# Kernel optimization log

Hardware: AMD Instinct MI355X
Metric: run time of the kernel (lower is better)

Reference implementation:

```python
import jax, jax.numpy as jnp
import numpy as np

D_MODEL = 512
NHEAD = 8
HEAD_DIM = D_MODEL // NHEAD
A, B = 1024, 16


def setup_inputs() -> dict:
    key = jax.random.key(0)
    ks = jax.random.split(key, 6)
    s = 1.0 / np.sqrt(D_MODEL)
    return {
        "src": jax.random.normal(ks[0], (A, B, D_MODEL), jnp.float32),
        "asset_relation_bias": jax.random.normal(ks[1], (A, A), jnp.float32) * 0.1,
        "Wq": jax.random.normal(ks[2], (D_MODEL, D_MODEL), jnp.float32) * s,
        "bq": jnp.zeros((D_MODEL,), jnp.float32),
        "Wk": jax.random.normal(ks[3], (D_MODEL, D_MODEL), jnp.float32) * s,
        "bk": jnp.zeros((D_MODEL,), jnp.float32),
        "Wv": jax.random.normal(ks[4], (D_MODEL, D_MODEL), jnp.float32) * s,
        "bv": jnp.zeros((D_MODEL,), jnp.float32),
        "Wo": jax.random.normal(ks[5], (D_MODEL, D_MODEL), jnp.float32) * s,
        "bo": jnp.zeros((D_MODEL,), jnp.float32),
    }


def reference(src, asset_relation_bias, Wq, bq, Wk, bk, Wv, bv, Wo, bo):
    # src: [A, B, H]; attention is over the asset dim A.
    scale = HEAD_DIM ** -0.5

    def proj_heads(x, W, b):
        y = x @ W.T + b                      # [A, B, H]  (torch Linear: x @ W.T + b)
        y = y.reshape(A, B, NHEAD, HEAD_DIM)
        return jnp.transpose(y, (1, 2, 0, 3))  # [B, nh, A, hd]

    q = proj_heads(src, Wq, bq)
    k = proj_heads(src, Wk, bk)
    v = proj_heads(src, Wv, bv)

    logits = jnp.einsum("bnad,bnkd->bnak", q, k) * scale  # [B, nh, A, A]
    logits = logits + asset_relation_bias[None, None]     # additive relation bias
    attn = jax.nn.softmax(logits, axis=-1)                # dropout = identity (eval)
    out = jnp.einsum("bnak,bnkd->bnad", attn, v)          # [B, nh, A, hd]
    out = jnp.transpose(out, (2, 0, 1, 3)).reshape(A, B, D_MODEL)
    out = out @ Wo.T + bo
    return out
```

## Files before the change

kernel.cpp:

```cpp
#include <hip/hip_runtime.h>
#include <hip/hip_bf16.h>

#define A_DIM 1024
#define B_DIM 16
#define DM    512
#define NH    8
#define HD    64

#define LDT 72

typedef short s16x8 __attribute__((ext_vector_type(8)));
typedef float f32x4 __attribute__((ext_vector_type(4)));

static __device__ __forceinline__ unsigned short f2b(float f) {
    __hip_bfloat16 h = __float2bfloat16(f);
    unsigned short u;
    __builtin_memcpy(&u, &h, 2);
    return u;
}
static __device__ __forceinline__ uint2 cvt4(float4 v) {
    __hip_bfloat162 lo = __float22bfloat162_rn(make_float2(v.x, v.y));
    __hip_bfloat162 hi = __float22bfloat162_rn(make_float2(v.z, v.w));
    unsigned int ulo, uhi;
    __builtin_memcpy(&ulo, &lo, 4);
    __builtin_memcpy(&uhi, &hi, 4);
    return make_uint2(ulo, uhi);
}

static __device__ __forceinline__ void gl_lds16(const short* g, short* l) {
    __builtin_amdgcn_global_load_lds(
        (const __attribute__((address_space(1))) unsigned int*)g,
        (__attribute__((address_space(3))) unsigned int*)l, 16, 0, 0);
}

__global__ __launch_bounds__(256) void cvt_src(
    const float* __restrict__ in, short* __restrict__ out)
{
    int i = (blockIdx.x * 256 + threadIdx.x) * 8;
    float4 a = *(const float4*)&in[i];
    float4 b = *(const float4*)&in[i + 4];
    *(uint2*)&out[i]     = cvt4(a);
    *(uint2*)&out[i + 4] = cvt4(b);
}

__global__ __launch_bounds__(256) void cvt_w(
    const float* __restrict__ Wq, const float* __restrict__ Wk,
    const float* __restrict__ Wv, const float* __restrict__ Wo,
    short* __restrict__ Wall)
{
    int i = blockIdx.x * 256 + threadIdx.x;
    int mat = i >> 15;
    const float* W = (mat == 0) ? Wq : (mat == 1) ? Wk : (mat == 2) ? Wv : Wo;
    int j = (i & 32767) * 8;
    float4 a = *(const float4*)&W[j];
    float4 b = *(const float4*)&W[j + 4];
    *(uint2*)&Wall[mat * (DM * DM) + j]     = cvt4(a);
    *(uint2*)&Wall[mat * (DM * DM) + j + 4] = cvt4(b);
}

__global__ __launch_bounds__(256) void qkv_gemm_bf(
    const short* __restrict__ Sb, const short* __restrict__ Wall,
    const float* __restrict__ bq, const float* __restrict__ bk,
    const float* __restrict__ bv,
    short* __restrict__ Qb, short* __restrict__ Kb, short* __restrict__ Vb)
{
    __shared__ __align__(16) short As[128 * 64];
    __shared__ __align__(16) short Bs[128 * 64];

    const int tid  = threadIdx.x;
    const int wave = tid >> 6, lane = tid & 63;
    const int quad = lane >> 4, l16 = lane & 15;
    const int waveM = (wave >> 1) * 64, waveN = (wave & 1) * 64;
    const int mbase = blockIdx.y * 128;
    const int nbase = blockIdx.x * 128;
    const int mat   = nbase >> 9;
    const short* Wm   = Wall + mat * (DM * DM);
    const float* bvec = (mat == 0) ? bq : (mat == 1) ? bk : bv;
    short* dst        = (mat == 0) ? Qb : (mat == 1) ? Kb : Vb;
    const float oscale = (mat == 0) ? 0.125f : 1.0f;
    const int wrow0 = nbase & 511;

    const int srow = lane >> 3;
    const int scol = (lane & 7) ^ srow;
    const int cxa  = l16 & 7;

    f32x4 acc[4][4];
    #pragma unroll
    for (int i = 0; i < 4; i++)
        #pragma unroll
        for (int j = 0; j < 4; j++)
            acc[i][j] = (f32x4){0.f, 0.f, 0.f, 0.f};

    for (int kb = 0; kb < 8; ++kb) {
        __syncthreads();
        #pragma unroll
        for (int p = 0; p < 4; p++) {
            int ch = wave + p * 4;
            int r  = ch * 8 + srow;
            gl_lds16(&Sb[(mbase + r) * 512 + kb * 64 + scol * 8],
                     &As[ch * 8 * 64]);
            gl_lds16(&Wm[(wrow0 + r) * 512 + kb * 64 + scol * 8],
                     &Bs[ch * 8 * 64]);
        }
        __syncthreads();
        #pragma unroll
        for (int k0i = 0; k0i < 2; k0i++) {
            s16x8 af[4], bf[4];
            #pragma unroll
            for (int mi = 0; mi < 4; mi++)
                af[mi] = *(const s16x8*)&As[(waveM + mi * 16 + l16) * 64
                                            + (((k0i * 4 + quad) ^ cxa) * 8)];
            #pragma unroll
            for (int ni = 0; ni < 4; ni++)
                bf[ni] = *(const s16x8*)&Bs[(waveN + ni * 16 + l16) * 64
                                            + (((k0i * 4 + quad) ^ cxa) * 8)];
            #pragma unroll
            for (int mi = 0; mi < 4; mi++)
                #pragma unroll
                for (int ni = 0; ni < 4; ni++)
                    acc[mi][ni] = __builtin_amdgcn_mfma_f32_16x16x32_bf16(
                        af[mi], bf[ni], acc[mi][ni], 0, 0, 0);
        }
    }

    #pragma unroll
    for (int mi = 0; mi < 4; mi++) {
        #pragma unroll
        for (int ni = 0; ni < 4; ni++) {
            #pragma unroll
            for (int r = 0; r < 4; r++) {
                int t = mbase + waveM + mi * 16 + quad * 4 + r;
                int o = wrow0 + waveN + ni * 16 + l16;
                float v = (acc[mi][ni][r] + bvec[o]) * oscale;
                int a = t >> 4, bb = t & 15, n = o >> 6, d = o & 63;
                dst[((bb * NH + n) * A_DIM + a) * HD + d] = (short)f2b(v);
            }
        }
    }
}

__global__ __launch_bounds__(256) void qkv_gemm(
    const float* __restrict__ src,
    const float* __restrict__ Wq, const float* __restrict__ bq,
    const float* __restrict__ Wk, const float* __restrict__ bk,
    const float* __restrict__ Wv, const float* __restrict__ bv,
    short* __restrict__ Qb, short* __restrict__ Kb, short* __restrict__ Vb)
{
    __shared__ short As[128 * LDT];
    __shared__ short Bs[128 * LDT];

    const int tid  = threadIdx.x;
    const int wave = tid >> 6, lane = tid & 63;
    const int quad = lane >> 4, l16 = lane & 15;
    const int waveM = (wave >> 1) * 64, waveN = (wave & 1) * 64;
    const int mbase = blockIdx.y * 128;
    const int nbase = blockIdx.x * 128;
    const int mat   = nbase >> 9;
    const float* W    = (mat == 0) ? Wq : (mat == 1) ? Wk : Wv;
    const float* bvec = (mat == 0) ? bq : (mat == 1) ? bk : bv;
    short* dst        = (mat == 0) ? Qb : (mat == 1) ? Kb : Vb;
    const float oscale = (mat == 0) ? 0.125f : 1.0f;
    const int wrow0 = nbase & 511;

    f32x4 acc[4][4];
    #pragma unroll
    for (int i = 0; i < 4; i++)
        #pragma unroll
        for (int j = 0; j < 4; j++)
            acc[i][j] = (f32x4){0.f, 0.f, 0.f, 0.f};

    for (int kb = 0; kb < 8; ++kb) {
        __syncthreads();
        #pragma unroll
        for (int p = 0; p < 8; p++) {
            int chunk = tid + p * 256;
            int row = chunk >> 4, c = chunk & 15;
            float4 a4 = *(const float4*)&src[(mbase + row) * 512 + kb * 64 + c * 4];
            *(uint2*)&As[row * LDT + c * 4] = cvt4(a4);
            float4 w4 = *(const float4*)&W[(wrow0 + row) * 512 + kb * 64 + c * 4];
            *(uint2*)&Bs[row * LDT + c * 4] = cvt4(w4);
        }
        __syncthreads();
        #pragma unroll
        for (int k0i = 0; k0i < 2; k0i++) {
            s16x8 af[4], bf[4];
            #pragma unroll
            for (int mi = 0; mi < 4; mi++)
                af[mi] = *(const s16x8*)&As[(waveM + mi * 16 + l16) * LDT + (k0i * 4 + quad) * 8];
            #pragma unroll
            for (int ni = 0; ni < 4; ni++)
                bf[ni] = *(const s16x8*)&Bs[(waveN + ni * 16 + l16) * LDT + (k0i * 4 + quad) * 8];
            #pragma unroll
            for (int mi = 0; mi < 4; mi++)
                #pragma unroll
                for (int ni = 0; ni < 4; ni++)
                    acc[mi][ni] = __builtin_amdgcn_mfma_f32_16x16x32_bf16(
                        af[mi], bf[ni], acc[mi][ni], 0, 0, 0);
        }
    }

    #pragma unroll
    for (int mi = 0; mi < 4; mi++) {
        #pragma unroll
        for (int ni = 0; ni < 4; ni++) {
            #pragma unroll
            for (int r = 0; r < 4; r++) {
                int t = mbase + waveM + mi * 16 + quad * 4 + r;
                int o = wrow0 + waveN + ni * 16 + l16;
                float v = (acc[mi][ni][r] + bvec[o]) * oscale;
                int a = t >> 4, bb = t & 15, n = o >> 6, d = o & 63;
                dst[((bb * NH + n) * A_DIM + a) * HD + d] = (short)f2b(v);
            }
        }
    }
}

__global__ __launch_bounds__(256) void attn_kernel(
    const short* __restrict__ Qb, const short* __restrict__ Kb,
    const short* __restrict__ Vb, const float* __restrict__ bias,
    short* __restrict__ AO)
{
    __shared__ short Ks[64 * LDT];
    __shared__ short Vt[64 * LDT];
    __shared__ short Ps[4][16 * LDT];

    const int tid  = threadIdx.x;
    const int wave = tid >> 6, lane = tid & 63;
    const int quad = lane >> 4, l16 = lane & 15;
    const int bn = blockIdx.y;
    const int qrow0 = blockIdx.x * 64 + wave * 16;

    const short* Qg = Qb + bn * (A_DIM * HD);
    const short* Kg = Kb + bn * (A_DIM * HD);
    const short* Vg = Vb + bn * (A_DIM * HD);

    s16x8 qf[2];
    #pragma unroll
    for (int k0i = 0; k0i < 2; k0i++)
        qf[k0i] = *(const s16x8*)&Qg[(qrow0 + l16) * HD + k0i * 32 + quad * 8];

    float lsum[4];
    f32x4 of[4];
    #pragma unroll
    for (int r = 0; r < 4; r++) lsum[r] = 0.f;
    #pragma unroll
    for (int db = 0; db < 4; db++) of[db] = (f32x4){0.f, 0.f, 0.f, 0.f};

    for (int kb = 0; kb < 16; ++kb) {
        __syncthreads();
        #pragma unroll
        for (int p = 0; p < 2; p++) {
            int chunk = tid + p * 256;
            int row = chunk >> 3, c = chunk & 7;
            *(s16x8*)&Ks[row * LDT + c * 8] =
                *(const s16x8*)&Kg[(kb * 64 + row) * HD + c * 8];
            s16x8 vv = *(const s16x8*)&Vg[(kb * 64 + row) * HD + c * 8];
            #pragma unroll
            for (int j = 0; j < 8; j++) {
                int d = c * 8 + j;
                Vt[d * LDT + (((row >> 3) ^ c) << 3) + (row & 7)] = vv[j];
            }
        }
        __syncthreads();

        float sv[4][4];
        #pragma unroll
        for (int cb = 0; cb < 4; cb++) {
            f32x4 s = (f32x4){0.f, 0.f, 0.f, 0.f};
            #pragma unroll
            for (int k0i = 0; k0i < 2; k0i++) {
                s16x8 kf = *(const s16x8*)&Ks[(cb * 16 + l16) * LDT + (k0i * 4 + quad) * 8];
                s = __builtin_amdgcn_mfma_f32_16x16x32_bf16(qf[k0i], kf, s, 0, 0, 0);
            }
            #pragma unroll
            for (int r = 0; r < 4; r++) {
                int arow = qrow0 + quad * 4 + r;
                int kcol = kb * 64 + cb * 16 + l16;
                sv[cb][r] = s[r] + bias[arow * A_DIM + kcol];
            }
        }

        #pragma unroll
        for (int r = 0; r < 4; r++) {
            int prow = quad * 4 + r;
            #pragma unroll
            for (int cb = 0; cb < 4; cb++) {
                float pv = __expf(sv[cb][r]);
                lsum[r] += pv;
                Ps[wave][prow * LDT + cb * 16 + l16] = (short)f2b(pv);
            }
        }

        #pragma unroll
        for (int k0i = 0; k0i < 2; k0i++) {
            s16x8 pf = *(const s16x8*)&Ps[wave][l16 * LDT + (k0i * 4 + quad) * 8];
            #pragma unroll
            for (int db = 0; db < 4; db++) {
                int rr = db * 16 + l16;
                s16x8 vf = *(const s16x8*)&Vt[rr * LDT +
                            (((k0i * 4 + quad) ^ (rr >> 3)) << 3)];
                of[db] = __builtin_amdgcn_mfma_f32_16x16x32_bf16(pf, vf, of[db], 0, 0, 0);
            }
        }
    }

    #pragma unroll
    for (int r = 0; r < 4; r++) {
        float ps = lsum[r];
        ps += __shfl_xor(ps, 1);
        ps += __shfl_xor(ps, 2);
        ps += __shfl_xor(ps, 4);
        ps += __shfl_xor(ps, 8);
        lsum[r] = 1.0f / ps;
    }

    const int b = bn >> 3, n = bn & 7;
    #pragma unroll
    for (int db = 0; db < 4; db++) {
        #pragma unroll
        for (int r = 0; r < 4; r++) {
            int a = qrow0 + quad * 4 + r;
            int d = db * 16 + l16;
            float v = of[db][r] * lsum[r];
            AO[(a * B_DIM + b) * DM + n * HD + d] = (short)f2b(v);
        }
    }
}

__global__ __launch_bounds__(256) void out_gemm_bf(
    const short* __restrict__ Xin,
    const short* __restrict__ Wob, const float* __restrict__ bo,
    float* __restrict__ out)
{
    __shared__ __align__(16) short As[128 * 64];
    __shared__ __align__(16) short Bs[128 * 64];

    const int tid  = threadIdx.x;
    const int wave = tid >> 6, lane = tid & 63;
    const int quad = lane >> 4, l16 = lane & 15;
    const int waveM = (wave >> 1) * 64, waveN = (wave & 1) * 64;
    const int mbase = blockIdx.y * 128;
    const int nbase = blockIdx.x * 128;

    const int srow = lane >> 3;
    const int scol = (lane & 7) ^ srow;
    const int cxa  = l16 & 7;

    f32x4 acc[4][4];
    #pragma unroll
    for (int i = 0; i < 4; i++)
        #pragma unroll
        for (int j = 0; j < 4; j++)
            acc[i][j] = (f32x4){0.f, 0.f, 0.f, 0.f};

    for (int kb = 0; kb < 8; ++kb) {
        __syncthreads();
        #pragma unroll
        for (int p = 0; p < 4; p++) {
            int ch = wave + p * 4;
            int r  = ch * 8 + srow;
            gl_lds16(&Xin[(mbase + r) * 512 + kb * 64 + scol * 8],
                     &As[ch * 8 * 64]);
            gl_lds16(&Wob[(nbase + r) * 512 + kb * 64 + scol * 8],
                     &Bs[ch * 8 * 64]);
        }
        __syncthreads();
        #pragma unroll
        for (int k0i = 0; k0i < 2; k0i++) {
            s16x8 af[4], bf[4];
            #pragma unroll
            for (int mi = 0; mi < 4; mi++)
                af[mi] = *(const s16x8*)&As[(waveM + mi * 16 + l16) * 64
                                            + (((k0i * 4 + quad) ^ cxa) * 8)];
            #pragma unroll
            for (int ni = 0; ni < 4; ni++)
                bf[ni] = *(const s16x8*)&Bs[(waveN + ni * 16 + l16) * 64
                                            + (((k0i * 4 + quad) ^ cxa) * 8)];
            #pragma unroll
            for (int mi = 0; mi < 4; mi++)
                #pragma unroll
                for (int ni = 0; ni < 4; ni++)
                    acc[mi][ni] = __builtin_amdgcn_mfma_f32_16x16x32_bf16(
                        af[mi], bf[ni], acc[mi][ni], 0, 0, 0);
        }
    }

    #pragma unroll
    for (int mi = 0; mi < 4; mi++) {
        #pragma unroll
        for (int ni = 0; ni < 4; ni++) {
            #pragma unroll
            for (int r = 0; r < 4; r++) {
                int t = mbase + waveM + mi * 16 + quad * 4 + r;
                int o = nbase + waveN + ni * 16 + l16;
                out[t * 512 + o] = acc[mi][ni][r] + bo[o];
            }
        }
    }
}

__global__ __launch_bounds__(256) void out_gemm(
    const short* __restrict__ Xin,
    const float* __restrict__ Wo, const float* __restrict__ bo,
    float* __restrict__ out)
{
    __shared__ short As[128 * LDT];
    __shared__ short Bs[128 * LDT];

    const int tid  = threadIdx.x;
    const int wave = tid >> 6, lane = tid & 63;
    const int quad = lane >> 4, l16 = lane & 15;
    const int waveM = (wave >> 1) * 64, waveN = (wave & 1) * 64;
    const int mbase = blockIdx.y * 128;
    const int nbase = blockIdx.x * 128;

    f32x4 acc[4][4];
    #pragma unroll
    for (int i = 0; i < 4; i++)
        #pragma unroll
        for (int j = 0; j < 4; j++)
            acc[i][j] = (f32x4){0.f, 0.f, 0.f, 0.f};

    for (int kb = 0; kb < 8; ++kb) {
        __syncthreads();
        #pragma unroll
        for (int p = 0; p < 4; p++) {
            int chunk = tid + p * 256;
            int row = chunk >> 3, c = chunk & 7;
            *(s16x8*)&As[row * LDT + c * 8] =
                *(const s16x8*)&Xin[(mbase + row) * 512 + kb * 64 + c * 8];
        }
        #pragma unroll
        for (int p = 0; p < 8; p++) {
            int chunk = tid + p * 256;
            int row = chunk >> 4, c = chunk & 15;
            float4 w4 = *(const float4*)&Wo[(nbase + row) * 512 + kb * 64 + c * 4];
            *(uint2*)&Bs[row * LDT + c * 4] = cvt4(w4);
        }
        __syncthreads();
        #pragma unroll
        for (int k0i = 0; k0i < 2; k0i++) {
            s16x8 af[4], bf[4];
            #pragma unroll
            for (int mi = 0; mi < 4; mi++)
                af[mi] = *(const s16x8*)&As[(waveM + mi * 16 + l16) * LDT + (k0i * 4 + quad) * 8];
            #pragma unroll
            for (int ni = 0; ni < 4; ni++)
                bf[ni] = *(const s16x8*)&Bs[(waveN + ni * 16 + l16) * LDT + (k0i * 4 + quad) * 8];
            #pragma unroll
            for (int mi = 0; mi < 4; mi++)
                #pragma unroll
                for (int ni = 0; ni < 4; ni++)
                    acc[mi][ni] = __builtin_amdgcn_mfma_f32_16x16x32_bf16(
                        af[mi], bf[ni], acc[mi][ni], 0, 0, 0);
        }
    }

    #pragma unroll
    for (int mi = 0; mi < 4; mi++) {
        #pragma unroll
        for (int ni = 0; ni < 4; ni++) {
            #pragma unroll
            for (int r = 0; r < 4; r++) {
                int t = mbase + waveM + mi * 16 + quad * 4 + r;
                int o = nbase + waveN + ni * 16 + l16;
                out[t * 512 + o] = acc[mi][ni][r] + bo[o];
            }
        }
    }
}

extern "C" void kernel_launch(void* const* d_in, const int* in_sizes, int n_in,
                              void* d_out, int out_size, void* d_ws, size_t ws_size,
                              hipStream_t stream) {
    const float* src  = (const float*)d_in[0];
    const float* bias = (const float*)d_in[1];
    const float* Wq   = (const float*)d_in[2];
    const float* bq   = (const float*)d_in[3];
    const float* Wk   = (const float*)d_in[4];
    const float* bk   = (const float*)d_in[5];
    const float* Wv   = (const float*)d_in[6];
    const float* bv   = (const float*)d_in[7];
    const float* Wo   = (const float*)d_in[8];
    const float* bo   = (const float*)d_in[9];

    short* ws = (short*)d_ws;
    short* Qb = ws;
    short* Kb = ws + (size_t)(1 << 23);
    short* Vb = ws + (size_t)(2 << 23);

    const bool big2   = ws_size >= (size_t)(66u << 20);
    const bool big_ws = ws_size >= (size_t)(64u << 20);

    if (big2) {
        short* Sb   = ws + (size_t)3 * (1 << 23);
        short* Wall = ws + (size_t)4 * (1 << 23);
        short* AO   = Sb;

        cvt_src<<<dim3(4096), 256, 0, stream>>>(src, Sb);
        cvt_w<<<dim3(512), 256, 0, stream>>>(Wq, Wk, Wv, Wo, Wall);
        qkv_gemm_bf<<<dim3(12, 128), 256, 0, stream>>>(Sb, Wall, bq, bk, bv, Qb, Kb, Vb);
        attn_kernel<<<dim3(16, 128), 256, 0, stream>>>(Qb, Kb, Vb, bias, AO);
        out_gemm_bf<<<dim3(4, 128), 256, 0, stream>>>(AO, Wall + 3 * (DM * DM), bo,
                                                      (float*)d_out);
    } else {
        short* AO = big_ws ? (ws + (size_t)3 * (1 << 23))
                           : (short*)d_out;

        qkv_gemm<<<dim3(12, 128), 256, 0, stream>>>(src, Wq, bq, Wk, bk, Wv, bv, Qb, Kb, Vb);
        attn_kernel<<<dim3(16, 128), 256, 0, stream>>>(Qb, Kb, Vb, bias, AO);

        if (big_ws) {
            out_gemm<<<dim3(4, 128), 256, 0, stream>>>(AO, Wo, bo, (float*)d_out);
        } else {
            float* Cs = (float*)d_ws;
            out_gemm<<<dim3(4, 128), 256, 0, stream>>>(AO, Wo, bo, Cs);
            (void)hipMemcpyAsync(d_out, Cs, (size_t)out_size * sizeof(float),
                                 hipMemcpyDeviceToDevice, stream);
        }
    }
}
```

Before: 241.8 us.

## Pre-transpose V and double-buffer K/V tiles in attention kernel

Adds a v_tr kernel that transposes V into a [bn, d, a] layout, using the output buffer as scratch. A new attention kernel reads the transposed V and double-buffers K and V shared-memory tiles. The next tile is prefetched into registers while the current one is computed, so there is one barrier per iteration. This aims to hide global load latency and simplify V staging, at the cost of an extra launch and a full extra read and write of V.

```diff
diff --git a/kernel.cpp b/kernel.cpp
--- a/kernel.cpp
+++ b/kernel.cpp
@@ -56,6 +56,30 @@
     float4 b = *(const float4*)&W[j + 4];
     *(uint2*)&Wall[mat * (DM * DM) + j]     = cvt4(a);
     *(uint2*)&Wall[mat * (DM * DM) + j + 4] = cvt4(b);
+}
+
+__global__ __launch_bounds__(256) void v_tr(
+    const short* __restrict__ V, short* __restrict__ Vt)
+{
+    __shared__ short t[64][74];
+    const int bn = blockIdx.y, a0 = blockIdx.x * 64;
+    const int rr = threadIdx.x >> 3, c = threadIdx.x & 7;
+
+    #pragma unroll
+    for (int h = 0; h < 2; h++) {
+        int a = rr + h * 32;
+        *(s16x8*)&t[a][c * 8] =
+            *(const s16x8*)&V[((size_t)bn * A_DIM + a0 + a) * HD + c * 8];
+    }
+    __syncthreads();
+    #pragma unroll
+    for (int h = 0; h < 2; h++) {
+        int d = rr + h * 32;
+        s16x8 y;
+        #pragma unroll
+        for (int j = 0; j < 8; j++) y[j] = t[c * 8 + j][d];
+        *(s16x8*)&Vt[((size_t)bn * HD + d) * A_DIM + a0 + c * 8] = y;
+    }
 }
 
 __global__ __launch_bounds__(256) void qkv_gemm_bf(
@@ -211,6 +235,138 @@
                 int a = t >> 4, bb = t & 15, n = o >> 6, d = o & 63;
                 dst[((bb * NH + n) * A_DIM + a) * HD + d] = (short)f2b(v);
             }
+        }
+    }
+}
+
+__global__ __launch_bounds__(256) void attn_kernel2(
+    const short* __restrict__ Qb, const short* __restrict__ Kb,
+    const short* __restrict__ Vtg, const float* __restrict__ bias,
+    short* __restrict__ AO)
+{
+    __shared__ short Ks[2][64 * LDT];
+    __shared__ short Vt[2][64 * LDT];
+    __shared__ short Ps[4][16 * LDT];
+
+    const int tid  = threadIdx.x;
+    const int wave = tid >> 6, lane = tid & 63;
+    const int quad = lane >> 4, l16 = lane & 15;
+    const int bn = blockIdx.y;
+    const int qrow0 = blockIdx.x * 64 + wave * 16;
+
+    const short* Qg = Qb  + bn * (A_DIM * HD);
+    const short* Kg = Kb  + bn * (A_DIM * HD);
+    const short* Vg = Vtg + bn * (HD * A_DIM);
+
+    s16x8 qf[2];
+    #pragma unroll
+    for (int k0i = 0; k0i < 2; k0i++)
+        qf[k0i] = *(const s16x8*)&Qg[(qrow0 + l16) * HD + k0i * 32 + quad * 8];
+
+    const int srow = tid >> 3, sc = tid & 7;
+
+    float lsum[4];
+    f32x4 of[4];
+    #pragma unroll
+    for (int r = 0; r < 4; r++) lsum[r] = 0.f;
+    #pragma unroll
+    for (int db = 0; db < 4; db++) of[db] = (f32x4){0.f, 0.f, 0.f, 0.f};
+
+    s16x8 kpre[2], vpre[2];
+    #pragma unroll
+    for (int p = 0; p < 2; p++) {
+        kpre[p] = *(const s16x8*)&Kg[(srow + p * 32) * HD + sc * 8];
+        vpre[p] = *(const s16x8*)&Vg[(srow + p * 32) * A_DIM + sc * 8];
+    }
+    #pragma unroll
+    for (int p = 0; p < 2; p++) {
+        int row = srow + p * 32;
+        *(s16x8*)&Ks[0][row * LDT + sc * 8] = kpre[p];
+        *(s16x8*)&Vt[0][row * LDT + ((sc ^ (wave + p * 4)) << 3)] = vpre[p];
+    }
+
+    int cur = 0;
+    for (int kb = 0; kb < 16; ++kb) {
+        __syncthreads();
+
+        if (kb < 15) {
+            #pragma unroll
+            for (int p = 0; p < 2; p++) {
+                kpre[p] = *(const s16x8*)&Kg[((kb + 1) * 64 + srow + p * 32) * HD + sc * 8];
+                vpre[p] = *(const s16x8*)&Vg[(srow + p * 32) * A_DIM + (kb + 1) * 64 + sc * 8];
+            }
+        }
+
+        float sv[4][4];
+        #pragma unroll
+        for (int cb = 0; cb < 4; cb++) {
+            f32x4 s = (f32x4){0.f, 0.f, 0.f, 0.f};
+            #pragma unroll
+            for (int k0i = 0; k0i < 2; k0i++) {
+                s16x8 kf = *(const s16x8*)&Ks[cur][(cb * 16 + l16) * LDT + (k0i * 4 + quad) * 8];
+                s = __builtin_amdgcn_mfma_f32_16x16x32_bf16(qf[k0i], kf, s, 0, 0, 0);
+            }
+            #pragma unroll
+            for (int r = 0; r < 4; r++) {
+                int arow = qrow0 + quad * 4 + r;
+                int kcol = kb * 64 + cb * 16 + l16;
+                sv[cb][r] = s[r] + bias[arow * A_DIM + kcol];
+            }
+        }
+
+        #pragma unroll
+        for (int r = 0; r < 4; r++) {
+            int prow = quad * 4 + r;
+            #pragma unroll
+            for (int cb = 0; cb < 4; cb++) {
+                float pv = __expf(sv[cb][r]);
+                lsum[r] += pv;
+                Ps[wave][prow * LDT + cb * 16 + l16] = (short)f2b(pv);
+            }
+        }
+
+        #pragma unroll
+        for (int k0i = 0; k0i < 2; k0i++) {
+            s16x8 pf = *(const s16x8*)&Ps[wave][l16 * LDT + (k0i * 4 + quad) * 8];
+            #pragma unroll
+            for (int db = 0; db < 4; db++) {
+                int rr = db * 16 + l16;
+                s16x8 vf = *(const s16x8*)&Vt[cur][rr * LDT +
+                            (((k0i * 4 + quad) ^ (rr >> 3)) << 3)];
+                of[db] = __builtin_amdgcn_mfma_f32_16x16x32_bf16(pf, vf, of[db], 0, 0, 0);
+            }
+        }
+
+        if (kb < 15) {
+            #pragma unroll
+            for (int p = 0; p < 2; p++) {
+                int row = srow + p * 32;
+                *(s16x8*)&Ks[cur ^ 1][row * LDT + sc * 8] = kpre[p];
+                *(s16x8*)&Vt[cur ^ 1][row * LDT + ((sc ^ (wave + p * 4)) << 3)] = vpre[p];
+            }
+        }
+        cur ^= 1;
+    }
+
+    #pragma unroll
+    for (int r = 0; r < 4; r++) {
+        float ps = lsum[r];
+        ps += __shfl_xor(ps, 1);
+        ps += __shfl_xor(ps, 2);
+        ps += __shfl_xor(ps, 4);
+        ps += __shfl_xor(ps, 8);
+        lsum[r] = 1.0f / ps;
+    }
+
+    const int b = bn >> 3, n = bn & 7;
+    #pragma unroll
+    for (int db = 0; db < 4; db++) {
+        #pragma unroll
+        for (int r = 0; r < 4; r++) {
+            int a = qrow0 + quad * 4 + r;
+            int d = db * 16 + l16;
+            float v = of[db][r] * lsum[r];
+            AO[(a * B_DIM + b) * DM + n * HD + d] = (short)f2b(v);
         }
     }
 }
@@ -496,11 +652,13 @@
         short* Sb   = ws + (size_t)3 * (1 << 23);
         short* Wall = ws + (size_t)4 * (1 << 23);
         short* AO   = Sb;
+        short* Vtb  = (short*)d_out;
 
         cvt_src<<<dim3(4096), 256, 0, stream>>>(src, Sb);
         cvt_w<<<dim3(512), 256, 0, stream>>>(Wq, Wk, Wv, Wo, Wall);
         qkv_gemm_bf<<<dim3(12, 128), 256, 0, stream>>>(Sb, Wall, bq, bk, bv, Qb, Kb, Vb);
-        attn_kernel<<<dim3(16, 128), 256, 0, stream>>>(Qb, Kb, Vb, bias, AO);
+        v_tr<<<dim3(16, 128), 256, 0, stream>>>(Vb, Vtb);
+        attn_kernel2<<<dim3(16, 128), 256, 0, stream>>>(Qb, Kb, Vtb, bias, AO);
         out_gemm_bf<<<dim3(4, 128), 256, 0, stream>>>(AO, Wall + 3 * (DM * DM), bo,
                                                       (float*)d_out);
     } else {
```

New measurement: 241.5 us. About the same (-0.1%).
